# Performance work log

Measured on AMD Instinct MI355X. Metric: run time of the kernel, lower is better.

Reference implementation:

```python
import jax, jax.numpy as jnp
import numpy as np

B, C, K = 8, 32, 512


def setup_inputs() -> dict:
    key = jax.random.key(0)
    k1, k2, k3 = jax.random.split(key, 3)
    amplitude = jax.random.normal(k1, (B, C, K), dtype=jnp.float32)
    phase = jax.random.normal(k2, (B, C, K), dtype=jnp.float32)
    A = jax.random.normal(k3, (K, K), dtype=jnp.float32)
    w_amplitude = jnp.float32(0.5)
    w_phase = jnp.float32(0.5)
    return {"amplitude": amplitude, "phase": phase, "A": A,
            "w_amplitude": w_amplitude, "w_phase": w_phase}


def reference(amplitude, phase, A, w_amplitude, w_phase):
    # amplitude, phase: (B, C, K)
    # pairwise differences along the frequency axis -> (B, C, K, K)
    amp_diff = amplitude[..., :, None] - amplitude[..., None, :]
    ph_diff = phase[..., :, None] - phase[..., None, :]
    fused = w_amplitude * amp_diff + w_phase * ph_diff
    # einsum('dd,bxcd->bxcd', A, fused): scale last axis by diag(A)
    temp = fused * jnp.diagonal(A)
    # einsum('bxcd,bxcd->bcd'): sum of squares over channel axis x=C -> (B, K, K)
    dist = jnp.sum(temp * temp, axis=1)
    exp_dist = 1.0 / (dist + 1e-10)
    eye = jnp.eye(K, dtype=exp_dist.dtype)
    offdiag = 1.0 - eye
    exp_dist = exp_dist * offdiag
    exp_max = jax.lax.stop_gradient(jnp.max(exp_dist, axis=-1, keepdims=True))
    p = exp_dist / exp_max
    p = (p * offdiag + eye) * 0.99  # probabilities in (0, 0.99]
    # bernoulli gumbel-softmax (hard, tau=1) with straight-through estimator
    logit = jnp.log(p / (1.0 - p))          # log(p/(1-p)); other class is -logit
    logits = jnp.stack([logit, -logit], axis=-1)  # (B, K, K, 2)
    gkey = jax.random.key(42)
    u = jax.random.uniform(gkey, logits.shape, minval=1e-10, maxval=1.0)
    gumbel = -jnp.log(-jnp.log(u))
    y_soft = jax.nn.softmax(logits + gumbel, axis=-1)
    idx = jnp.argmax(y_soft, axis=-1)
    y_hard = jax.nn.one_hot(idx, 2, dtype=y_soft.dtype)
    y = y_hard + y_soft - jax.lax.stop_gradient(y_soft)
    sample = y[..., 0]  # (B, K, K)
    return sample.mean(axis=0)  # (K, K)
```

## Files before the change

kernel.cpp:

```cpp
#include <hip/hip_runtime.h>
#include <stdint.h>
#include <math.h>

constexpr int NB = 8;
constexpr int NC = 32;
constexpr int NK = 512;
constexpr int ROWS = 2;

__device__ __forceinline__ uint32_t rotl32(uint32_t x, uint32_t r) {
    return (x << r) | (x >> (32u - r));
}

__device__ __forceinline__ uint32_t jax_random_bits(uint32_t n) {
    const uint32_t k0 = 0u, k1 = 42u;
    const uint32_t ks2 = k0 ^ k1 ^ 0x1BD11BDAu;
    uint32_t x0 = 0u + k0, x1 = n + k1;

    x0 += x1; x1 = rotl32(x1, 13); x1 ^= x0;
    x0 += x1; x1 = rotl32(x1, 15); x1 ^= x0;
    x0 += x1; x1 = rotl32(x1, 26); x1 ^= x0;
    x0 += x1; x1 = rotl32(x1,  6); x1 ^= x0;
    x0 += k1; x1 += ks2 + 1u;

    x0 += x1; x1 = rotl32(x1, 17); x1 ^= x0;
    x0 += x1; x1 = rotl32(x1, 29); x1 ^= x0;
    x0 += x1; x1 = rotl32(x1, 16); x1 ^= x0;
    x0 += x1; x1 = rotl32(x1, 24); x1 ^= x0;
    x0 += ks2; x1 += k0 + 2u;

    x0 += x1; x1 = rotl32(x1, 13); x1 ^= x0;
    x0 += x1; x1 = rotl32(x1, 15); x1 ^= x0;
    x0 += x1; x1 = rotl32(x1, 26); x1 ^= x0;
    x0 += x1; x1 = rotl32(x1,  6); x1 ^= x0;
    x0 += k0; x1 += k1 + 3u;

    x0 += x1; x1 = rotl32(x1, 17); x1 ^= x0;
    x0 += x1; x1 = rotl32(x1, 29); x1 ^= x0;
    x0 += x1; x1 = rotl32(x1, 16); x1 ^= x0;
    x0 += x1; x1 = rotl32(x1, 24); x1 ^= x0;
    x0 += k1; x1 += ks2 + 4u;

    x0 += x1; x1 = rotl32(x1, 13); x1 ^= x0;
    x0 += x1; x1 = rotl32(x1, 15); x1 ^= x0;
    x0 += x1; x1 = rotl32(x1, 26); x1 ^= x0;
    x0 += x1; x1 = rotl32(x1,  6); x1 ^= x0;
    x0 += ks2; x1 += k0 + 5u;

    return x0 ^ x1;
}

__device__ __forceinline__ float fastL(uint32_t bits, double& ud) {
    const double S = 1.0 - 1e-10, T = 1e-10;
    uint32_t fb = (bits >> 9) | 0x3F800000u;
    float bf = __uint_as_float(fb) - 1.0f;
    ud = (double)bf * S + T;
    if (bf <= 0.5f) {
        return -logf((float)ud);
    } else {
        double vm1 = S * ((double)bf - 1.0);
        return -log1pf((float)vm1);
    }
}

__device__ __noinline__ bool decide_slow(double a2, double c2,
                                         double u0, double u1) {
    return a2 * (-log(u1)) >= c2 * (-log(u0));
}

__device__ __forceinline__ bool decide_rng(double D, double q ,
                                           bool diag, uint32_t n0) {
    double a2, c2;
    if (diag) { a2 = 9801.0; c2 = 1.0; }
    else      { a2 = q * q; double t = D - q; c2 = t * t; }

    uint32_t bits0 = jax_random_bits(n0);
    uint32_t bits1 = jax_random_bits(n0 + 1u);
    double u0d, u1d;
    float L0f = fastL(bits0, u0d);
    float L1f = fastL(bits1, u1d);

    float lhs = (float)a2 * L1f;
    float rhs = (float)c2 * L0f;
    float diff = lhs - rhs;
    if (fabsf(diff) > 1e-4f * (lhs + rhs))
        return diff >= 0.0f;
    return decide_slow(a2, c2, u0d, u1d);
}

__global__ void prep_kernel(const float* __restrict__ amp,
                            const float* __restrict__ ph,
                            const float* __restrict__ A,
                            const float* __restrict__ wav,
                            const float* __restrict__ wpv,
                            double* __restrict__ F,
                            double* __restrict__ A2,
                            float* __restrict__ out) {
    int t = blockIdx.x * 256 + threadIdx.x;
    out[t] = 0.0f;
    if (t < NB * NC * NK) {
        double wa = (double)wav[0], wp = (double)wpv[0];
        F[t] = wa * (double)amp[t] + wp * (double)ph[t];
    }
    if (t < NK) {
        double a = (double)A[t * NK + t];
        A2[t] = a * a;
    }
}

__global__ __launch_bounds__(256) void sample_kernel(
    const double* __restrict__ F, const double* __restrict__ A2,
    float* __restrict__ out)
{
    const int i0   = blockIdx.x * ROWS;
    const int b    = blockIdx.y;
    const int tid  = threadIdx.x;
    const int j0   = 2 * tid;
    const int lane = tid & 63;
    const int wv   = tid >> 6;
    const int wjb  = wv * 128;

    __shared__ unsigned char wlist[4][ROWS][128];
    __shared__ double sred[ROWS][4];
    __shared__ double s_q[ROWS];

    const double* __restrict__ Fb = F + (size_t)b * NC * NK;

    double acc[2][ROWS];
    #pragma unroll
    for (int it = 0; it < 2; ++it)
        #pragma unroll
        for (int r = 0; r < ROWS; ++r) acc[it][r] = 0.0;

    #pragma unroll 4
    for (int c = 0; c < NC; ++c) {
        double fr0 = Fb[c * NK + i0];
        double fr1 = Fb[c * NK + i0 + 1];
        double2 fj = *(const double2*)(Fb + c * NK + j0);
        double d00 = fr0 - fj.x; acc[0][0] = fma(d00, d00, acc[0][0]);
        double d10 = fr0 - fj.y; acc[1][0] = fma(d10, d10, acc[1][0]);
        double d01 = fr1 - fj.x; acc[0][1] = fma(d01, d01, acc[0][1]);
        double d11 = fr1 - fj.y; acc[1][1] = fma(d11, d11, acc[1][1]);
    }

    double2 a2j = *(const double2*)(A2 + j0);
    double D[2][ROWS];
    #pragma unroll
    for (int r = 0; r < ROWS; ++r) {
        D[0][r] = acc[0][r] * a2j.x + 1e-10;
        D[1][r] = acc[1][r] * a2j.y + 1e-10;
    }

    #pragma unroll
    for (int r = 0; r < ROWS; ++r) {
        const int i = i0 + r;
        double m = 1e300;
        if (j0     != i) m = fmin(m, D[0][r]);
        if (j0 + 1 != i) m = fmin(m, D[1][r]);
        #pragma unroll
        for (int off = 32; off > 0; off >>= 1)
            m = fmin(m, __shfl_down(m, off));
        if (lane == 0) sred[r][wv] = m;
    }
    __syncthreads();
    if (tid < ROWS) {
        double m = fmin(fmin(sred[tid][0], sred[tid][1]),
                        fmin(sred[tid][2], sred[tid][3]));
        s_q[tid] = 0.99 * m;
    }
    __syncthreads();

    const unsigned long long ltmask = (1ull << lane) - 1ull;
    int nw[ROWS];
    #pragma unroll
    for (int r = 0; r < ROWS; ++r) {
        const int i = i0 + r;
        const double q = s_q[r];
        const double thr = 1.95e8 * (q * q);
        double t0 = D[0][r] - q;
        double t1 = D[1][r] - q;
        bool need0 = (j0     == i) || !(t0 * t0 > thr);
        bool need1 = (j0 + 1 == i) || !(t1 * t1 > thr);
        unsigned long long m0 = __ballot(need0);
        unsigned long long m1 = __ballot(need1);
        int c0 = __popcll(m0);
        nw[r] = c0 + __popcll(m1);
        if (need0) wlist[wv][r][__popcll(m0 & ltmask)]      = (unsigned char)(2 * lane);
        if (need1) wlist[wv][r][c0 + __popcll(m1 & ltmask)] = (unsigned char)(2 * lane + 1);
    }

    #pragma unroll
    for (int r = 0; r < ROWS; ++r) {
        const int i = i0 + r;
        const double q = s_q[r];
        const int n = nw[r];
        for (int k0v = 0; k0v < n; k0v += 64) {
            int k = k0v + lane;
            bool act = k < n;
            int jl = wlist[wv][r][act ? k : 0];
            int src = jl >> 1;
            double d0s = __shfl(D[0][r], src);
            double d1s = __shfl(D[1][r], src);
            double Dv = (jl & 1) ? d1s : d0s;
            int j = wjb + jl;
            uint32_t n0 = 2u * (((uint32_t)(b * NK + i)) * NK + (uint32_t)j);
            if (act && decide_rng(Dv, q, j == i, n0))
                atomicAdd(&out[i * NK + j], 0.125f);
        }
    }
}

extern "C" void kernel_launch(void* const* d_in, const int* in_sizes, int n_in,
                              void* d_out, int out_size, void* d_ws, size_t ws_size,
                              hipStream_t stream) {
    const float* amp = (const float*)d_in[0];
    const float* ph  = (const float*)d_in[1];
    const float* A   = (const float*)d_in[2];
    const float* wa  = (const float*)d_in[3];
    const float* wp  = (const float*)d_in[4];
    float* out = (float*)d_out;

    double* F  = (double*)d_ws;
    double* A2 = (double*)d_ws + NB * NC * NK;

    prep_kernel<<<1024, 256, 0, stream>>>(amp, ph, A, wa, wp, F, A2, out);

    dim3 grid(NK / ROWS, NB);
    sample_kernel<<<grid, 256, 0, stream>>>(F, A2, out);
}
```

Before: 84.92 us.

## Process four rows per block and skip second RNG draw when first decides

Each block now handles four query rows instead of two, so every column value loaded from F is reused across more rows and the grid shrinks by half. The RNG decision is inlined and first computes only the first Threefry draw. If c2*L0 already exceeds the largest possible a2*L1 (bounded by about 23.03, since u is at least 1e-10), the sample is rejected and the second draw is skipped. The trade-off is more registers and fewer blocks per launch, plus a bound that depends on the clamp in fastL being correct.

After: 85.12 us. No clear change (+0.2%).

```diff
diff --git a/kernel.cpp b/kernel.cpp
--- a/kernel.cpp
+++ b/kernel.cpp
@@ -5,7 +5,7 @@
 constexpr int NB = 8;
 constexpr int NC = 32;
 constexpr int NK = 512;
-constexpr int ROWS = 2;
+constexpr int ROWS = 4;
 
 __device__ __forceinline__ uint32_t rotl32(uint32_t x, uint32_t r) {
     return (x << r) | (x >> (32u - r));
@@ -65,26 +65,6 @@
 __device__ __noinline__ bool decide_slow(double a2, double c2,
                                          double u0, double u1) {
     return a2 * (-log(u1)) >= c2 * (-log(u0));
-}
-
-__device__ __forceinline__ bool decide_rng(double D, double q ,
-                                           bool diag, uint32_t n0) {
-    double a2, c2;
-    if (diag) { a2 = 9801.0; c2 = 1.0; }
-    else      { a2 = q * q; double t = D - q; c2 = t * t; }
-
-    uint32_t bits0 = jax_random_bits(n0);
-    uint32_t bits1 = jax_random_bits(n0 + 1u);
-    double u0d, u1d;
-    float L0f = fastL(bits0, u0d);
-    float L1f = fastL(bits1, u1d);
-
-    float lhs = (float)a2 * L1f;
-    float rhs = (float)c2 * L0f;
-    float diff = lhs - rhs;
-    if (fabsf(diff) > 1e-4f * (lhs + rhs))
-        return diff >= 0.0f;
-    return decide_slow(a2, c2, u0d, u1d);
 }
 
 __global__ void prep_kernel(const float* __restrict__ amp,
@@ -131,15 +111,18 @@
         #pragma unroll
         for (int r = 0; r < ROWS; ++r) acc[it][r] = 0.0;
 
-    #pragma unroll 4
+    #pragma unroll 8
     for (int c = 0; c < NC; ++c) {
-        double fr0 = Fb[c * NK + i0];
-        double fr1 = Fb[c * NK + i0 + 1];
+        double fi_r[ROWS];
+        #pragma unroll
+        for (int r = 0; r < ROWS; ++r)
+            fi_r[r] = Fb[c * NK + i0 + r];
         double2 fj = *(const double2*)(Fb + c * NK + j0);
-        double d00 = fr0 - fj.x; acc[0][0] = fma(d00, d00, acc[0][0]);
-        double d10 = fr0 - fj.y; acc[1][0] = fma(d10, d10, acc[1][0]);
-        double d01 = fr1 - fj.x; acc[0][1] = fma(d01, d01, acc[0][1]);
-        double d11 = fr1 - fj.y; acc[1][1] = fma(d11, d11, acc[1][1]);
+        #pragma unroll
+        for (int r = 0; r < ROWS; ++r) {
+            double d0 = fi_r[r] - fj.x; acc[0][r] = fma(d0, d0, acc[0][r]);
+            double d1 = fi_r[r] - fj.y; acc[1][r] = fma(d1, d1, acc[1][r]);
+        }
     }
 
     double2 a2j = *(const double2*)(A2 + j0);
@@ -202,8 +185,32 @@
             double d1s = __shfl(D[1][r], src);
             double Dv = (jl & 1) ? d1s : d0s;
             int j = wjb + jl;
+
+            double a2, c2;
+            if (j == i) { a2 = 9801.0; c2 = 1.0; }
+            else        { a2 = q * q; double t = Dv - q; c2 = t * t; }
+
             uint32_t n0 = 2u * (((uint32_t)(b * NK + i)) * NK + (uint32_t)j);
-            if (act && decide_rng(Dv, q, j == i, n0))
+            bool hit = false;
+            if (act) {
+                uint32_t bits0 = jax_random_bits(n0);
+                double u0d;
+                float L0f = fastL(bits0, u0d);
+                float L0lo = L0f * 0.99999f;
+                if (!((double)c2 * (double)L0lo > 23.03 * a2)) {
+                    uint32_t bits1 = jax_random_bits(n0 + 1u);
+                    double u1d;
+                    float L1f = fastL(bits1, u1d);
+                    float lhs = (float)a2 * L1f;
+                    float rhs = (float)c2 * L0f;
+                    float diff = lhs - rhs;
+                    if (fabsf(diff) > 1e-4f * (lhs + rhs))
+                        hit = diff >= 0.0f;
+                    else
+                        hit = decide_slow(a2, c2, u0d, u1d);
+                }
+            }
+            if (hit)
                 atomicAdd(&out[i * NK + j], 0.125f);
         }
     }
```
